# Optimization experiments

Hardware: AMD Instinct MI355X
Metric: run time of the kernel (lower is better)

## Reference

```python
import jax, jax.numpy as jnp
import numpy as np

B, S, E, H = 2, 4096, 512, 8
DK = E // H


def setup_inputs() -> dict:
    k = jax.random.key(0)
    ks = jax.random.split(k, 11)
    sc = 0.02
    return {
        "query": jax.random.normal(ks[0], (B, S, E), jnp.float32),
        "key_in": jax.random.normal(ks[1], (B, S, E), jnp.float32),
        "value": jax.random.normal(ks[2], (B, S, E), jnp.float32),
        "Wq": jax.random.normal(ks[3], (E, E), jnp.float32) * sc,
        "bq": jax.random.normal(ks[4], (E,), jnp.float32) * sc,
        "Wk": jax.random.normal(ks[5], (E, E), jnp.float32) * sc,
        "bk": jax.random.normal(ks[6], (E,), jnp.float32) * sc,
        "Wv": jax.random.normal(ks[7], (E, E), jnp.float32) * sc,
        "bv": jax.random.normal(ks[8], (E,), jnp.float32) * sc,
        "Wo": jax.random.normal(ks[9], (E, E), jnp.float32) * sc,
        "bo": jax.random.normal(ks[10], (E,), jnp.float32) * sc,
    }


def reference(query, key_in, value, Wq, bq, Wk, bk, Wv, bv, Wo, bo):
    b, s, _ = query.shape
    # Linear projections
    q = query @ Wq + bq
    k = key_in @ Wk + bk
    v = value @ Wv + bv
    # [b, s, H, dk] -> [b, H, s, dk]
    q = q.reshape(b, s, H, DK).transpose(0, 2, 1, 3)
    k = k.reshape(b, s, H, DK).transpose(0, 2, 1, 3)
    v = v.reshape(b, s, H, DK).transpose(0, 2, 1, 3)
    # NOTE: source bug — softmax over UNSCALED scores (1/sqrt scaling in the
    # original is applied to a dead variable after softmax). Reproduce faithfully.
    scores = jnp.einsum("bhqd,bhkd->bhqk", q, k)  # [b,H,s,s] — O(N^2) materialized
    weights = jax.nn.softmax(scores.astype(jnp.float32), axis=-1)
    attn = jnp.einsum("bhqk,bhkd->bhqd", weights, v)
    # [b,H,s,dk] -> [b,s,E]
    concat = attn.transpose(0, 2, 1, 3).reshape(b, s, E)
    return concat @ Wo + bo
```

## Files before the change

kernel.cpp:

```cpp
#include <hip/hip_runtime.h>
#include <hip/hip_bf16.h>

#define B_  2
#define S_  4096
#define E_  512
#define H_  8
#define DK_ 64
#define M_  8192

typedef float f32x4  __attribute__((ext_vector_type(4)));
typedef float f32x16 __attribute__((ext_vector_type(16)));
typedef short s16x8  __attribute__((ext_vector_type(8)));
typedef short s16x4  __attribute__((ext_vector_type(4)));

static __device__ __forceinline__ short f2bf(float x) {
  __hip_bfloat16 h = __float2bfloat16(x);
  return __builtin_bit_cast(short, h);
}

static __device__ __forceinline__ f32x4 mfma32(s16x8 a, s16x8 b, f32x4 c) {
  return __builtin_amdgcn_mfma_f32_16x16x32_bf16(a, b, c, 0, 0, 0);
}

static __device__ __forceinline__ f32x16 mfma3232(s16x8 a, s16x8 b, f32x16 c) {
  return __builtin_amdgcn_mfma_f32_32x32x16_bf16(a, b, c, 0, 0, 0);
}

static __device__ __forceinline__ float fastexp2(float x) {
#if __has_builtin(__builtin_amdgcn_exp2f)
  return __builtin_amdgcn_exp2f(x);
#else
  return __expf(x * 0.69314718056f);
#endif
}

static __device__ __forceinline__ void gload_lds16(const void* g, void* l) {
  __builtin_amdgcn_global_load_lds(
      (const __attribute__((address_space(1))) unsigned int*)g,
      (__attribute__((address_space(3))) unsigned int*)l, 16, 0, 0);
}

__global__ __launch_bounds__(256) void conv_bf16_all(
    const float* __restrict__ q, const float* __restrict__ k,
    const float* __restrict__ v, short* __restrict__ out, int n4) {
  const float* in = (blockIdx.y == 0) ? q : ((blockIdx.y == 1) ? k : v);
  short* o = out + (size_t)blockIdx.y * (size_t)n4 * 4;
  int i = blockIdx.x * 256 + threadIdx.x;
  if (i < n4) {
    float4 x = *((const float4*)in + i);
    s16x4 r;
    r[0] = f2bf(x.x); r[1] = f2bf(x.y); r[2] = f2bf(x.z); r[3] = f2bf(x.w);
    *((s16x4*)o + i) = r;
  }
}

__global__ __launch_bounds__(256) void conv_wT_all(
    const float* __restrict__ Wq, const float* __restrict__ Wk,
    const float* __restrict__ Wv, const float* __restrict__ Wo,
    short* __restrict__ Wt) {
  const float* W = (blockIdx.y == 0) ? Wq
                   : ((blockIdx.y == 1) ? Wk : ((blockIdx.y == 2) ? Wv : Wo));
  short* o = Wt + (size_t)blockIdx.y * (E_ * E_);
  int idx = blockIdx.x * 256 + threadIdx.x;
  int j = idx >> 9, k = idx & 511;
  o[idx] = f2bf(W[(size_t)k * E_ + j]);
}

static __device__ __forceinline__ void gemm_core_512(
    const short* __restrict__ A, const short* __restrict__ Bt,
    short* As, short* Bs, int tm, int tn, f32x4 acc[4][4]) {
  const int tid = threadIdx.x;
  const int wave = tid >> 6, lane = tid & 63;
  const int wm = (wave >> 1) * 64, wn = (wave & 1) * 64;
  const int c = lane & 15, g = lane >> 4;
  for (int kk = 0; kk < 512; kk += 64) {
#pragma unroll
    for (int i = 0; i < 4; ++i) {
      int ob = wave * 4096 + i * 1024 + lane * 16;
      int row = ob >> 7;
      int col = (ob & 127) >> 1;
      gload_lds16(A + (size_t)(tm + row) * 512 + kk + col,
                  (char*)As + wave * 4096 + i * 1024);
      gload_lds16(Bt + (size_t)(tn + row) * 512 + kk + col,
                  (char*)Bs + wave * 4096 + i * 1024);
    }
    __syncthreads();
#pragma unroll
    for (int s = 0; s < 2; ++s) {
      s16x8 af[4], bfr[4];
#pragma unroll
      for (int i = 0; i < 4; ++i)
        af[i] = *(const s16x8*)&As[(wm + i * 16 + c) * 64 + s * 32 + g * 8];
#pragma unroll
      for (int j = 0; j < 4; ++j)
        bfr[j] = *(const s16x8*)&Bs[(wn + j * 16 + c) * 64 + s * 32 + g * 8];
#pragma unroll
      for (int i = 0; i < 4; ++i)
#pragma unroll
        for (int j = 0; j < 4; ++j)
          acc[i][j] = mfma32(af[i], bfr[j], acc[i][j]);
    }
    __syncthreads();
  }
}

__global__ __launch_bounds__(256) void gemm_qkv(
    const short* __restrict__ Xq, const short* __restrict__ Xk,
    const short* __restrict__ Xv, const short* __restrict__ Wt,
    const float* __restrict__ bq, const float* __restrict__ bk,
    const float* __restrict__ bv,
    short* __restrict__ Qo, short* __restrict__ Ko, short* __restrict__ Vto) {
  __shared__ __align__(16) short As[128 * 64];
  __shared__ __align__(16) short Bs[128 * 64];
  const int z = blockIdx.z;
  const short* A = (z == 0) ? Xq : ((z == 1) ? Xk : Xv);
  const short* Bt = Wt + z * (E_ * E_);
  const float* bias = (z == 0) ? bq : ((z == 1) ? bk : bv);
  const int tm = blockIdx.x * 128, tn = blockIdx.y * 128;
  f32x4 acc[4][4] = {};
  gemm_core_512(A, Bt, As, Bs, tm, tn, acc);

  const int tid = threadIdx.x;
  const int wave = tid >> 6, lane = tid & 63;
  const int wm = (wave >> 1) * 64, wn = (wave & 1) * 64;
  const int c = lane & 15, g = lane >> 4;
#pragma unroll
  for (int i = 0; i < 4; ++i) {
#pragma unroll
    for (int j = 0; j < 4; ++j) {
      const int gc = tn + wn + j * 16 + c;
      const float bb = bias[gc];
      const int h = gc >> 6, dk = gc & 63;
#pragma unroll
      for (int r = 0; r < 4; ++r) {
        const int gr = tm + wm + i * 16 + g * 4 + r;
        const int b = gr >> 12, s = gr & 4095;
        float v = acc[i][j][r] + bb;
        if (z == 0) v *= 1.44269504f;
        const short hv = f2bf(v);
        if (z == 2)
          Vto[(size_t)((b * H_ + h) * DK_ + dk) * S_ + s] = hv;
        else if (z == 1)
          Ko[(size_t)((b * H_ + h) * S_ + s) * DK_ + dk] = hv;
        else
          Qo[(size_t)((b * H_ + h) * S_ + s) * DK_ + dk] = hv;
      }
    }
  }
}

__global__ __launch_bounds__(256) void gemm_out(
    const short* __restrict__ AO, const short* __restrict__ Wot,
    const float* __restrict__ bo, float* __restrict__ out) {
  __shared__ __align__(16) short As[128 * 64];
  __shared__ __align__(16) short Bs[128 * 64];
  const int tm = blockIdx.x * 128, tn = blockIdx.y * 128;
  f32x4 acc[4][4] = {};
  gemm_core_512(AO, Wot, As, Bs, tm, tn, acc);

  const int tid = threadIdx.x;
  const int wave = tid >> 6, lane = tid & 63;
  const int wm = (wave >> 1) * 64, wn = (wave & 1) * 64;
  const int c = lane & 15, g = lane >> 4;
#pragma unroll
  for (int i = 0; i < 4; ++i) {
#pragma unroll
    for (int j = 0; j < 4; ++j) {
      const int gc = tn + wn + j * 16 + c;
      const float bb = bo[gc];
#pragma unroll
      for (int r = 0; r < 4; ++r) {
        const int gr = tm + wm + i * 16 + g * 4 + r;
        out[(size_t)gr * E_ + gc] = acc[i][j][r] + bb;
      }
    }
  }
}

__global__ __launch_bounds__(512, 2) void attn_fwd(
    const short* __restrict__ Q, const short* __restrict__ K,
    const short* __restrict__ Vt, short* __restrict__ O) {
  __shared__ __align__(16) char lds[49152];
  const int tid = threadIdx.x;
  const int wave = tid >> 6, lane = tid & 63;
  const int g = wave >> 1, kh = wave & 1;
  const int qi = lane & 31, hi = lane >> 5;
  const int bh = blockIdx.y;
  const int b = bh >> 3, h = bh & 7;
  const int q0 = blockIdx.x * 256 + g * 64;
  const short* Qp = Q + (size_t)bh * S_ * DK_;
  const short* Kp = K + (size_t)bh * S_ * DK_;
  const short* Vp = Vt + (size_t)bh * DK_ * S_;

  s16x8 qfL[4], qfH[4];
#pragma unroll
  for (int s = 0; s < 4; ++s) {
    qfL[s] = *(const s16x8*)(Qp + (size_t)(q0 + qi) * DK_ + s * 16 + hi * 8);
    qfH[s] = *(const s16x8*)(Qp + (size_t)(q0 + 32 + qi) * DK_ + s * 16 + hi * 8);
  }

  f32x16 o00 = {}, o01 = {}, o10 = {}, o11 = {};
  float lsL = 0.f, lsH = 0.f;

  int kOff, vOff;
  {
    const int j = wave;
    const int row = (j >> 2) * 32 + qi;
    const int srow = (row & 32) | ((row & 8) << 1) | ((row & 4) << 1) |
                     ((row & 16) >> 2) | (row & 3);
    kOff = srow * DK_ + (j & 3) * 16 + hi * 8;
    vOff = ((j >> 2) * 32 + qi) * S_ + ((j >> 1) & 1) * 32 +
           (j & 1) * 16 + hi * 8;
  }

  auto stage = [&](int kt) {
    gload_lds16(Kp + (size_t)kt * 64 * DK_ + kOff,
                lds + (kt % 3) * 8192 + wave * 1024);
    gload_lds16(Vp + (size_t)kt * 64 + vOff,
                lds + 24576 + (kt % 3) * 8192 + wave * 1024);
  };

  auto bar2 = [&]() {
    asm volatile("s_waitcnt vmcnt(2) lgkmcnt(0)" ::: "memory");
    __builtin_amdgcn_s_barrier();
  };
  auto bar0 = [&]() {
    asm volatile("s_waitcnt vmcnt(0) lgkmcnt(0)" ::: "memory");
    __builtin_amdgcn_s_barrier();
  };

  const int lbK = kh * 4096 + (lane << 4);

  auto qk = [&](int t, f32x16& sL, f32x16& sH) {
    const char* Kc = lds + (t % 3) * 8192 + lbK;
    f32x16 a = {}, c = {};
    __builtin_amdgcn_s_setprio(1);
#pragma unroll
    for (int s = 0; s < 4; ++s) {
      s16x8 ka = *(const s16x8*)(Kc + s * 1024);
      a = mfma3232(ka, qfL[s], a);
      c = mfma3232(ka, qfH[s], c);
    }
    __builtin_amdgcn_s_setprio(0);
    sL = a; sH = c;
  };

  auto softpv = [&](const f32x16& sL, const f32x16& sH, int t) {
    const char* Vc = lds + 24576 + (t % 3) * 8192 + kh * 2048 + (lane << 4);
    float pL[16], pH[16];
#pragma unroll
    for (int r = 0; r < 16; ++r) { pL[r] = fastexp2(sL[r]); pH[r] = fastexp2(sH[r]); }
    float aL = 0.f, aH = 0.f;
#pragma unroll
    for (int r = 0; r < 16; ++r) { aL += pL[r]; aH += pH[r]; }
    lsL += aL; lsH += aH;
    s16x8 pbL[2], pbH[2];
#pragma unroll
    for (int ks = 0; ks < 2; ++ks)
#pragma unroll
      for (int j = 0; j < 8; ++j) {
        const int r = (j & 3) | (ks << 2) | ((j >> 2) << 3);
        pbL[ks][j] = f2bf(pL[r]);
        pbH[ks][j] = f2bf(pH[r]);
      }
    __builtin_amdgcn_s_setprio(1);
#pragma unroll
    for (int ks = 0; ks < 2; ++ks) {
      s16x8 va0 = *(const s16x8*)(Vc + ks * 1024);
      s16x8 va1 = *(const s16x8*)(Vc + 4096 + ks * 1024);
      o00 = mfma3232(va0, pbL[ks], o00);
      o01 = mfma3232(va0, pbH[ks], o01);
      o10 = mfma3232(va1, pbL[ks], o10);
      o11 = mfma3232(va1, pbH[ks], o11);
    }
    __builtin_amdgcn_s_setprio(0);
  };

  const int NT = S_ / 64;
  f32x16 sA0, sA1, sB0, sB1;

  stage(0);
  stage(1);
  bar2();
  qk(0, sA0, sA1);

  for (int t = 0; t < NT; t += 2) {
    if (t + 2 < NT) { stage(t + 2); bar2(); } else { bar0(); }
    qk(t + 1, sB0, sB1);
    softpv(sA0, sA1, t);
    if (t + 3 < NT) { stage(t + 3); bar2(); } else { bar0(); }
    if (t + 2 < NT) qk(t + 2, sA0, sA1);
    softpv(sB0, sB1, t + 1);
  }

  lsL += __shfl_xor(lsL, 32);
  lsH += __shfl_xor(lsH, 32);

  float* mrg = (float*)lds;
  const int mi = (g * 64 + lane) * 36;
  __syncthreads();
  if (kh) {
#pragma unroll
    for (int r = 0; r < 4; ++r) {
      *(f32x4*)(mrg + mi + r * 4) =
          f32x4{o00[r * 4], o00[r * 4 + 1], o00[r * 4 + 2], o00[r * 4 + 3]};
      *(f32x4*)(mrg + mi + 16 + r * 4) =
          f32x4{o01[r * 4], o01[r * 4 + 1], o01[r * 4 + 2], o01[r * 4 + 3]};
    }
    mrg[mi + 32] = lsL;
    mrg[mi + 33] = lsH;
  }
  __syncthreads();
  float rlL = 0.f, rlH = 0.f;
  if (!kh) {
#pragma unroll
    for (int r = 0; r < 16; ++r) {
      o00[r] += mrg[mi + r];
      o01[r] += mrg[mi + 16 + r];
    }
    rlL = 1.f / (lsL + mrg[mi + 32]);
    rlH = 1.f / (lsH + mrg[mi + 33]);
  }
  __syncthreads();
  if (kh) {
#pragma unroll
    for (int r = 0; r < 4; ++r) {
      *(f32x4*)(mrg + mi + r * 4) =
          f32x4{o10[r * 4], o10[r * 4 + 1], o10[r * 4 + 2], o10[r * 4 + 3]};
      *(f32x4*)(mrg + mi + 16 + r * 4) =
          f32x4{o11[r * 4], o11[r * 4 + 1], o11[r * 4 + 2], o11[r * 4 + 3]};
    }
  }
  __syncthreads();
  if (!kh) {
#pragma unroll
    for (int r = 0; r < 16; ++r) {
      o10[r] += mrg[mi + r];
      o11[r] += mrg[mi + 16 + r];
    }
    short* OpL = O + ((size_t)(b * S_ + q0 + qi)) * E_ + h * DK_;
    short* OpH = O + ((size_t)(b * S_ + q0 + 32 + qi)) * E_ + h * DK_;
#pragma unroll
    for (int rr = 0; rr < 4; ++rr) {
      s16x4 vL0, vL1, vH0, vH1;
#pragma unroll
      for (int e = 0; e < 4; ++e) {
        vL0[e] = f2bf(o00[rr * 4 + e] * rlL);
        vL1[e] = f2bf(o10[rr * 4 + e] * rlL);
        vH0[e] = f2bf(o01[rr * 4 + e] * rlH);
        vH1[e] = f2bf(o11[rr * 4 + e] * rlH);
      }
      *(s16x4*)(OpL + rr * 8 + hi * 4) = vL0;
      *(s16x4*)(OpL + 32 + rr * 8 + hi * 4) = vL1;
      *(s16x4*)(OpH + rr * 8 + hi * 4) = vH0;
      *(s16x4*)(OpH + 32 + rr * 8 + hi * 4) = vH1;
    }
  }
}

extern "C" void kernel_launch(void* const* d_in, const int* in_sizes, int n_in,
                              void* d_out, int out_size, void* d_ws, size_t ws_size,
                              hipStream_t stream) {
  const float* query  = (const float*)d_in[0];
  const float* key_in = (const float*)d_in[1];
  const float* value  = (const float*)d_in[2];
  const float* Wq = (const float*)d_in[3];
  const float* bq = (const float*)d_in[4];
  const float* Wk = (const float*)d_in[5];
  const float* bk = (const float*)d_in[6];
  const float* Wv = (const float*)d_in[7];
  const float* bv = (const float*)d_in[8];
  const float* Wo = (const float*)d_in[9];
  const float* bo = (const float*)d_in[10];
  float* out = (float*)d_out;

  const size_t NA = (size_t)M_ * E_;
  short* ws  = (short*)d_ws;
  short* Xq  = ws;
  short* Wt  = Xq + 3 * NA;
  short* Wot = Wt + 3 * E_ * E_;
  short* Qb  = Wt + 4 * E_ * E_;
  short* Kb  = Qb + NA;
  short* Vtb = Kb + NA;
  short* AO  = Vtb + NA;
  short* Xk  = Xq + NA;
  short* Xv  = Xk + NA;

  conv_bf16_all<<<dim3(NA / 1024, 3), 256, 0, stream>>>(
      query, key_in, value, Xq, (int)(NA / 4));
  conv_wT_all<<<dim3(E_ * E_ / 256, 4), 256, 0, stream>>>(Wq, Wk, Wv, Wo, Wt);

  gemm_qkv<<<dim3(M_ / 128, E_ / 128, 3), 256, 0, stream>>>(
      Xq, Xk, Xv, Wt, bq, bk, bv, Qb, Kb, Vtb);
  attn_fwd<<<dim3(S_ / 256, B_ * H_), 512, 0, stream>>>(Qb, Kb, Vtb, AO);
  gemm_out<<<dim3(M_ / 128, E_ / 128), 256, 0, stream>>>(AO, Wot, bo, out);
}
```

Measured before the change: 154.1 us.

## Double-buffer GEMM LDS tiles with fragment-ordered layout and vectorize V-transpose stores

The projection GEMM core now stages 32-wide K slices into two LDS buffers, prefetching the next slice while MFMAs run on the current one. Tiles are stored in per-fragment order so each lane reads its operand with one contiguous 16-byte load. The V-transpose epilogue writes four consecutive sequence positions as one packed store instead of four scalar stores. The goal is to hide global-load latency and improve LDS and store efficiency. The cost is one barrier per K step and twice as many loop iterations.

After: 148.0 us. 1.04x faster.

```diff
diff --git a/kernel.cpp b/kernel.cpp
--- a/kernel.cpp
+++ b/kernel.cpp
@@ -71,35 +71,41 @@
     short* As, short* Bs, int tm, int tn, f32x4 acc[4][4]) {
   const int tid = threadIdx.x;
   const int wave = tid >> 6, lane = tid & 63;
-  const int wm = (wave >> 1) * 64, wn = (wave & 1) * 64;
   const int c = lane & 15, g = lane >> 4;
-  for (int kk = 0; kk < 512; kk += 64) {
-#pragma unroll
-    for (int i = 0; i < 4; ++i) {
-      int ob = wave * 4096 + i * 1024 + lane * 16;
-      int row = ob >> 7;
-      int col = (ob & 127) >> 1;
-      gload_lds16(A + (size_t)(tm + row) * 512 + kk + col,
-                  (char*)As + wave * 4096 + i * 1024);
-      gload_lds16(Bt + (size_t)(tn + row) * 512 + kk + col,
-                  (char*)Bs + wave * 4096 + i * 1024);
-    }
-    __syncthreads();
-#pragma unroll
-    for (int s = 0; s < 2; ++s) {
-      s16x8 af[4], bfr[4];
-#pragma unroll
-      for (int i = 0; i < 4; ++i)
-        af[i] = *(const s16x8*)&As[(wm + i * 16 + c) * 64 + s * 32 + g * 8];
+  int fOff[2];
+#pragma unroll
+  for (int r = 0; r < 2; ++r) {
+    const int f = wave * 2 + r;
+    fOff[r] = ((f >> 2) * 64 + (f & 3) * 16 + c) * 512 + g * 8;
+  }
+  auto stg = [&](int p, int b) {
+#pragma unroll
+    for (int r = 0; r < 2; ++r) {
+      const int f = wave * 2 + r;
+      gload_lds16(A + (size_t)tm * 512 + p * 32 + fOff[r],
+                  (char*)As + b * 8192 + f * 1024);
+      gload_lds16(Bt + (size_t)tn * 512 + p * 32 + fOff[r],
+                  (char*)Bs + b * 8192 + f * 1024);
+    }
+  };
+  stg(0, 0);
+  __syncthreads();
+  for (int p = 0; p < 16; ++p) {
+    if (p + 1 < 16) stg(p + 1, (p + 1) & 1);
+    const short* Ac = As + (p & 1) * 4096;
+    const short* Bc = Bs + (p & 1) * 4096;
+    s16x8 af[4], bfr[4];
+#pragma unroll
+    for (int i = 0; i < 4; ++i)
+      af[i] = *(const s16x8*)(Ac + ((wave >> 1) * 4 + i) * 512 + lane * 8);
+#pragma unroll
+    for (int j = 0; j < 4; ++j)
+      bfr[j] = *(const s16x8*)(Bc + ((wave & 1) * 4 + j) * 512 + lane * 8);
+#pragma unroll
+    for (int i = 0; i < 4; ++i)
 #pragma unroll
       for (int j = 0; j < 4; ++j)
-        bfr[j] = *(const s16x8*)&Bs[(wn + j * 16 + c) * 64 + s * 32 + g * 8];
-#pragma unroll
-      for (int i = 0; i < 4; ++i)
-#pragma unroll
-        for (int j = 0; j < 4; ++j)
-          acc[i][j] = mfma32(af[i], bfr[j], acc[i][j]);
-    }
+        acc[i][j] = mfma32(af[i], bfr[j], acc[i][j]);
     __syncthreads();
   }
 }
@@ -110,8 +116,8 @@
     const float* __restrict__ bq, const float* __restrict__ bk,
     const float* __restrict__ bv,
     short* __restrict__ Qo, short* __restrict__ Ko, short* __restrict__ Vto) {
-  __shared__ __align__(16) short As[128 * 64];
-  __shared__ __align__(16) short Bs[128 * 64];
+  __shared__ __align__(16) short As[2 * 4096];
+  __shared__ __align__(16) short Bs[2 * 4096];
   const int z = blockIdx.z;
   const short* A = (z == 0) ? Xq : ((z == 1) ? Xk : Xv);
   const short* Bt = Wt + z * (E_ * E_);
@@ -131,19 +137,26 @@
       const int gc = tn + wn + j * 16 + c;
       const float bb = bias[gc];
       const int h = gc >> 6, dk = gc & 63;
-#pragma unroll
-      for (int r = 0; r < 4; ++r) {
-        const int gr = tm + wm + i * 16 + g * 4 + r;
-        const int b = gr >> 12, s = gr & 4095;
-        float v = acc[i][j][r] + bb;
-        if (z == 0) v *= 1.44269504f;
-        const short hv = f2bf(v);
-        if (z == 2)
-          Vto[(size_t)((b * H_ + h) * DK_ + dk) * S_ + s] = hv;
-        else if (z == 1)
-          Ko[(size_t)((b * H_ + h) * S_ + s) * DK_ + dk] = hv;
-        else
-          Qo[(size_t)((b * H_ + h) * S_ + s) * DK_ + dk] = hv;
+      if (z == 2) {
+        const int gr0 = tm + wm + i * 16 + g * 4;
+        const int b = gr0 >> 12, s0 = gr0 & 4095;
+        s16x4 v4;
+#pragma unroll
+        for (int r = 0; r < 4; ++r) v4[r] = f2bf(acc[i][j][r] + bb);
+        *(s16x4*)&Vto[(size_t)((b * H_ + h) * DK_ + dk) * S_ + s0] = v4;
+      } else {
+#pragma unroll
+        for (int r = 0; r < 4; ++r) {
+          const int gr = tm + wm + i * 16 + g * 4 + r;
+          const int b = gr >> 12, s = gr & 4095;
+          float v = acc[i][j][r] + bb;
+          if (z == 0) v *= 1.44269504f;
+          const short hv = f2bf(v);
+          if (z == 1)
+            Ko[(size_t)((b * H_ + h) * S_ + s) * DK_ + dk] = hv;
+          else
+            Qo[(size_t)((b * H_ + h) * S_ + s) * DK_ + dk] = hv;
+        }
       }
     }
   }
@@ -152,8 +165,8 @@
 __global__ __launch_bounds__(256) void gemm_out(
     const short* __restrict__ AO, const short* __restrict__ Wot,
     const float* __restrict__ bo, float* __restrict__ out) {
-  __shared__ __align__(16) short As[128 * 64];
-  __shared__ __align__(16) short Bs[128 * 64];
+  __shared__ __align__(16) short As[2 * 4096];
+  __shared__ __align__(16) short Bs[2 * 4096];
   const int tm = blockIdx.x * 128, tn = blockIdx.y * 128;
   f32x4 acc[4][4] = {};
   gemm_core_512(AO, Wot, As, Bs, tm, tn, acc);
```
